# Performance work log

Hardware: AMD Instinct MI355X
Metric: run time of the kernel (lower is better)

Reference implementation:

```python
import jax, jax.numpy as jnp
import numpy as np
import math

D_MODEL = 1024
D_ATTN = 128
D_MID = 128
L = 4096

def setup_inputs() -> dict:
    key = jax.random.key(0)
    ks = jax.random.split(key, 5)
    scale = 1.0 / math.sqrt(D_MODEL)
    return {
        "x": jax.random.normal(ks[0], (L, D_MODEL), jnp.float32),
        "z": jax.random.normal(ks[1], (L, D_MODEL), jnp.float32),
        "Wq": jax.random.normal(ks[2], (D_MODEL, D_ATTN), jnp.float32) * scale,
        "bq": jnp.zeros((D_ATTN,), jnp.float32),
        "Wk": jax.random.normal(ks[3], (D_MODEL, D_ATTN), jnp.float32) * scale,
        "bk": jnp.zeros((D_ATTN,), jnp.float32),
        "Wv": jax.random.normal(ks[4], (D_MODEL, D_MID), jnp.float32) * scale,
        "bv": jnp.zeros((D_MID,), jnp.float32),
    }

def reference(x, z, Wq, bq, Wk, bk, Wv, bv):
    # q: [L_x, d_attn], k: [L_z, d_attn], v: [L_z, d_mid]
    q = x @ Wq + bq
    k = z @ Wk + bk
    v = z @ Wv + bv
    inv_sqrt_d = 1.0 / math.sqrt(D_ATTN)
    s = (q @ k.T) * inv_sqrt_d            # [L_x, L_z]
    y = jax.nn.softmax(s, axis=-1) @ v    # [L_x, d_mid]
    return y
```

## Files before the change

kernel.cpp:

```cpp
#include <hip/hip_runtime.h>
#include <hip/hip_bf16.h>

typedef __attribute__((ext_vector_type(8))) short short8;
typedef __attribute__((ext_vector_type(4))) float f32x4;

#define L_SEQ 4096
#define DM    1024
#define DA    128
#define PS    2
#define AZ    8

#define OFF_QB  786432
#define OFF_KF  1835008
#define OFF_VF  2883584
#define OFF_SCR 4063232

__device__ __forceinline__ short f2bf(float f) {
    union { float f; unsigned u; } v; v.f = f;
    unsigned u = v.u;
    u += 0x7FFFu + ((u >> 16) & 1u);
    return (short)(u >> 16);
}

typedef const __attribute__((address_space(1))) void g_void_t;
typedef __attribute__((address_space(3))) void l_void_t;
__device__ __forceinline__ void g2lds16(const void* g, void* l) {
    __builtin_amdgcn_global_load_lds((g_void_t*)g, (l_void_t*)l, 16, 0, 0);
}

__global__ __launch_bounds__(256) void prep_w_kernel(
    const float* __restrict__ Wq, const float* __restrict__ Wk,
    const float* __restrict__ Wv, short8* __restrict__ WTf)
{
    const int m = blockIdx.y, kidx = blockIdx.x;
    const float* __restrict__ W = (m == 0) ? Wq : (m == 1) ? Wk : Wv;
    __shared__ __align__(16) float Ws[32 * 132];
    const int t = threadIdx.x;
#pragma unroll
    for (int i = 0; i < 4; i++) {
        const int u = i * 256 + t;
        const int kk = u >> 5, n4 = (u & 31) * 4;
        *(f32x4*)&Ws[kk * 132 + n4] = *(const f32x4*)&W[(size_t)(kidx * 32 + kk) * DA + n4];
    }
    __syncthreads();
#pragma unroll
    for (int i = 0; i < 2; i++) {
        const int u = i * 256 + t;
        const int nt = u >> 6, lane = u & 63, l16 = lane & 15, quad = lane >> 4;
        short8 fr;
#pragma unroll
        for (int j = 0; j < 8; j++)
            fr[j] = f2bf(Ws[(quad * 8 + j) * 132 + nt * 16 + l16]);
        WTf[((size_t)(m * 32 + kidx) * 8 + nt) * 64 + lane] = fr;
    }
}

__global__ __launch_bounds__(256, 1) void proj_kernel(
    const float* __restrict__ x, const float* __restrict__ z,
    const char* __restrict__ WTraw, float* __restrict__ part)
{
    __shared__ __align__(16) char wb[2][16384];

    const int t = threadIdx.x;
    const int wave = t >> 6, lane = t & 63;
    const int l16 = lane & 15, quad = lane >> 4;
    const int isKV = blockIdx.y;
    const int s = blockIdx.z;
    const int kbeg = s * (DM / PS);
    const int row0w = blockIdx.x * 64 + wave * 16;
    const int m1 = isKV ? 1 : 0;
    const int nbytes = isKV ? 16384 : 8192;
    const int ks0 = kbeg >> 5;

    const float* __restrict__ Am = isKV ? z : x;
    const float* ap = Am + (size_t)(row0w + l16) * DM + kbeg + quad * 8;

    f32x4 acc1[8], acc2[8];
#pragma unroll
    for (int i = 0; i < 8; i++) {
        acc1[i] = (f32x4){0.f, 0.f, 0.f, 0.f};
        acc2[i] = (f32x4){0.f, 0.f, 0.f, 0.f};
    }

    auto stage = [&](int kidx, int b) {
        const char* base1 = WTraw + (size_t)(m1 * 32 + kidx) * 8192;
        const char* base2 = WTraw + (size_t)(2 * 32 + kidx) * 8192;
#pragma unroll
        for (int i = 0; i < 4; i++) {
            const int off = i * 4096 + wave * 1024;
            if (off < nbytes) {
                const char* src = (off < 8192) ? (base1 + off) : (base2 + (off - 8192));
                g2lds16(src + lane * 16, &wb[b][off]);
            }
        }
    };

    f32x4 c0 = *(const f32x4*)ap,        c1 = *(const f32x4*)(ap + 4);
    f32x4 d0 = *(const f32x4*)(ap + 32), d1 = *(const f32x4*)(ap + 36);

    stage(ks0, 0);
    __syncthreads();

#pragma unroll 1
    for (int ks = 0; ks < 16; ks++) {
        const int b = ks & 1;
        if (ks + 1 < 16) stage(ks0 + ks + 1, b ^ 1);

        const int kpf = (ks + 2 < 16) ? ks + 2 : ks;
        f32x4 e0 = *(const f32x4*)(ap + kpf * 32);
        f32x4 e1 = *(const f32x4*)(ap + kpf * 32 + 4);

        short8 afr;
        afr[0] = f2bf(c0[0]); afr[1] = f2bf(c0[1]); afr[2] = f2bf(c0[2]); afr[3] = f2bf(c0[3]);
        afr[4] = f2bf(c1[0]); afr[5] = f2bf(c1[1]); afr[6] = f2bf(c1[2]); afr[7] = f2bf(c1[3]);

#pragma unroll
        for (int nt = 0; nt < 8; nt++) {
            short8 bfr = *(const short8*)&wb[b][(nt * 64 + lane) * 16];
            acc1[nt] = __builtin_amdgcn_mfma_f32_16x16x32_bf16(afr, bfr, acc1[nt], 0, 0, 0);
        }
        if (isKV) {
#pragma unroll
            for (int nt = 0; nt < 8; nt++) {
                short8 bfr = *(const short8*)&wb[b][8192 + (nt * 64 + lane) * 16];
                acc2[nt] = __builtin_amdgcn_mfma_f32_16x16x32_bf16(afr, bfr, acc2[nt], 0, 0, 0);
            }
        }
        __syncthreads();
        c0 = d0; c1 = d1; d0 = e0; d1 = e1;
    }

    float* p1 = part + (size_t)(s * 3 + m1) * L_SEQ * DA;
#pragma unroll
    for (int nt = 0; nt < 8; nt++) {
        const int col = nt * 16 + l16;
#pragma unroll
        for (int r = 0; r < 4; r++)
            p1[(size_t)(row0w + quad * 4 + r) * DA + col] = acc1[nt][r];
    }
    if (isKV) {
        float* p2 = part + (size_t)(s * 3 + 2) * L_SEQ * DA;
#pragma unroll
        for (int nt = 0; nt < 8; nt++) {
            const int col = nt * 16 + l16;
#pragma unroll
            for (int r = 0; r < 4; r++)
                p2[(size_t)(row0w + quad * 4 + r) * DA + col] = acc2[nt][r];
        }
    }
}

__global__ __launch_bounds__(256) void finalize_kernel(
    const float* __restrict__ part,
    const float* __restrict__ bq, const float* __restrict__ bk,
    const float* __restrict__ bv,
    short* __restrict__ qb, short8* __restrict__ kf, short8* __restrict__ vf)
{
    const int t = threadIdx.x;
    const int row0 = blockIdx.x * 32;
    __shared__ short Ts[DA * 33];

#pragma unroll 1
    for (int m = 0; m < 3; m++) {
        const float* __restrict__ bias = (m == 0) ? bq : (m == 1) ? bk : bv;
#pragma unroll
        for (int i = 0; i < 2; i++) {
            const int u = i * 256 + t;
            const int r = u >> 4, cg8 = u & 15;
            const int R = row0 + r, c0 = cg8 * 8;
            float vsum[8];
#pragma unroll
            for (int j = 0; j < 8; j++) vsum[j] = bias[c0 + j];
            for (int s = 0; s < PS; s++) {
                const float* p = &part[((size_t)(s * 3 + m) * L_SEQ + R) * DA + c0];
                f32x4 f0 = *(const f32x4*)p;
                f32x4 f1 = *(const f32x4*)(p + 4);
#pragma unroll
                for (int j = 0; j < 4; j++) { vsum[j] += f0[j]; vsum[4 + j] += f1[j]; }
            }
            short8 o;
#pragma unroll
            for (int j = 0; j < 8; j++) o[j] = f2bf(vsum[j]);

            if (m == 0) {
                *(short8*)&qb[(size_t)R * DA + c0] = o;
            } else if (m == 1) {
                const int kg = R >> 5, nth = (R >> 4) & 1, l16 = R & 15;
                const int ks = cg8 >> 2, quad = cg8 & 3;
                kf[((size_t)(kg * 4 + ks) * 2 + nth) * 64 + quad * 16 + l16] = o;
            } else {
#pragma unroll
                for (int j = 0; j < 8; j++) Ts[(c0 + j) * 33 + r] = o[j];
            }
        }
    }
    __syncthreads();

    const int vg = blockIdx.x;
#pragma unroll
    for (int i = 0; i < 3; i++) {
        const int u = i * 256 + t;
        if (u < 576) {
            const int nt = u >> 6, lane = u & 63, l16 = lane & 15, quad = lane >> 4;
            short8 fr;
            if (nt < 8) {
                const int col = nt * 16 + l16;
#pragma unroll
                for (int j = 0; j < 8; j++) fr[j] = Ts[col * 33 + quad * 8 + j];
            } else {
                const short one = (short)0x3F80;
#pragma unroll
                for (int j = 0; j < 8; j++) fr[j] = (l16 == 0) ? one : (short)0;
            }
            vf[((size_t)vg * 9 + nt) * 64 + lane] = fr;
        }
    }
}

__global__ __launch_bounds__(256, 1) void attn_kernel(
    const short* __restrict__ qb, const char* __restrict__ kfg,
    const char* __restrict__ vfg, float* __restrict__ OA,
    float* __restrict__ lA)
{
    __shared__ __align__(16) char kv[2][17408];
    __shared__ __align__(16) short Ps[4][2][16 * 40];

    const int t    = threadIdx.x;
    const int wave = t >> 6;
    const int lane = t & 63;
    const int l16  = lane & 15;
    const int quad = lane >> 4;
    const int qr0  = blockIdx.x * 128;
    const int g0   = blockIdx.y * 16;

    auto stage = [&](int g, int b) {
        const char* kb_ = kfg + (size_t)(g0 + g) * 8192;
        const char* vb_ = vfg + (size_t)(g0 + g) * 9216;
#pragma unroll
        for (int i = 0; i < 5; i++) {
            const int off = i * 4096 + wave * 1024;
            if (off < 17408) {
                const char* src = (off < 8192) ? (kb_ + off) : (vb_ + (off - 8192));
                g2lds16(src + lane * 16, &kv[b][off]);
            }
        }
    };

    stage(0, 0);

    short8 af[2][4];
    const short* qrow = qb + (size_t)(qr0 + wave * 32 + l16) * DA + quad * 8;
#pragma unroll
    for (int at = 0; at < 2; at++)
#pragma unroll
        for (int ks = 0; ks < 4; ks++)
            af[at][ks] = *(const short8*)(qrow + (size_t)at * 16 * DA + ks * 32);

    f32x4 O0[9], O1[9];
#pragma unroll
    for (int i = 0; i < 9; i++) {
        O0[i] = (f32x4){0.f, 0.f, 0.f, 0.f};
        O1[i] = (f32x4){0.f, 0.f, 0.f, 0.f};
    }

    const float C = 0.08838834764831845f;
    short* P0 = &Ps[wave][0][0];
    short* P1 = &Ps[wave][1][0];

    __syncthreads();

#pragma unroll 1
    for (int g = 0; g < 16; g++) {
        const int b = g & 1;
        if (g + 1 < 16) stage(g + 1, b ^ 1);

        const char* kb_ = &kv[b][0];
        const char* vb_ = &kv[b][8192];

        f32x4 s0[2], s1[2];
#pragma unroll
        for (int nh = 0; nh < 2; nh++) {
            s0[nh] = (f32x4){0.f, 0.f, 0.f, 0.f};
            s1[nh] = (f32x4){0.f, 0.f, 0.f, 0.f};
        }
#pragma unroll
        for (int nh = 0; nh < 2; nh++)
#pragma unroll
            for (int ks = 0; ks < 4; ks++) {
                short8 bfr = *(const short8*)(kb_ + ((ks * 2 + nh) * 64 + lane) * 16);
                s0[nh] = __builtin_amdgcn_mfma_f32_16x16x32_bf16(af[0][ks], bfr, s0[nh], 0, 0, 0);
                s1[nh] = __builtin_amdgcn_mfma_f32_16x16x32_bf16(af[1][ks], bfr, s1[nh], 0, 0, 0);
            }

#pragma unroll
        for (int nh = 0; nh < 2; nh++)
#pragma unroll
            for (int r = 0; r < 4; r++) {
                P0[(quad * 4 + r) * 40 + nh * 16 + l16] = f2bf(__expf(s0[nh][r] * C));
                P1[(quad * 4 + r) * 40 + nh * 16 + l16] = f2bf(__expf(s1[nh][r] * C));
            }
        asm volatile("" ::: "memory");
        __builtin_amdgcn_s_waitcnt(0xc07f);
        asm volatile("" ::: "memory");

        short8 a20 = *(const short8*)&P0[l16 * 40 + quad * 8];
        short8 a21 = *(const short8*)&P1[l16 * 40 + quad * 8];
#pragma unroll
        for (int nt = 0; nt < 9; nt++) {
            short8 b2 = *(const short8*)(vb_ + (nt * 64 + lane) * 16);
            O0[nt] = __builtin_amdgcn_mfma_f32_16x16x32_bf16(a20, b2, O0[nt], 0, 0, 0);
            O1[nt] = __builtin_amdgcn_mfma_f32_16x16x32_bf16(a21, b2, O1[nt], 0, 0, 0);
        }
        __syncthreads();
    }

    const int rw = qr0 + wave * 32;
    float* Ob = OA + (size_t)blockIdx.y * L_SEQ * DA;
#pragma unroll
    for (int nt = 0; nt < 8; nt++)
#pragma unroll
        for (int r = 0; r < 4; r++) {
            Ob[(size_t)(rw + quad * 4 + r) * DA + nt * 16 + l16] = O0[nt][r];
            Ob[(size_t)(rw + 16 + quad * 4 + r) * DA + nt * 16 + l16] = O1[nt][r];
        }
    if (l16 == 0) {
        float* lb = lA + (size_t)blockIdx.y * L_SEQ;
#pragma unroll
        for (int r = 0; r < 4; r++) {
            lb[rw + quad * 4 + r] = O0[8][r];
            lb[rw + 16 + quad * 4 + r] = O1[8][r];
        }
    }
}

__global__ __launch_bounds__(256) void merge_kernel(
    const float* __restrict__ OA, const float* __restrict__ lA,
    float* __restrict__ out)
{
    const int t = threadIdx.x;
    const int row = blockIdx.x * 16 + (t >> 4);
    const int cg = (t & 15) * 8;

    f32x4 a0 = (f32x4){0.f, 0.f, 0.f, 0.f};
    f32x4 a1 = (f32x4){0.f, 0.f, 0.f, 0.f};
    float lsum = 0.f;
#pragma unroll
    for (int zz = 0; zz < AZ; zz++) {
        const float* p = &OA[((size_t)zz * L_SEQ + row) * DA + cg];
        a0 = a0 + *(const f32x4*)p;
        a1 = a1 + *(const f32x4*)(p + 4);
        lsum += lA[(size_t)zz * L_SEQ + row];
    }
    const float inv = 1.f / lsum;
    f32x4* dst = (f32x4*)&out[(size_t)row * DA + cg];
    dst[0] = a0 * inv;
    dst[1] = a1 * inv;
}

extern "C" void kernel_launch(void* const* d_in, const int* in_sizes, int n_in,
                              void* d_out, int out_size, void* d_ws, size_t ws_size,
                              hipStream_t stream) {
    (void)in_sizes; (void)n_in; (void)out_size; (void)ws_size;
    const float* x  = (const float*)d_in[0];
    const float* z  = (const float*)d_in[1];
    const float* Wq = (const float*)d_in[2];
    const float* bq = (const float*)d_in[3];
    const float* Wk = (const float*)d_in[4];
    const float* bk = (const float*)d_in[5];
    const float* Wv = (const float*)d_in[6];
    const float* bv = (const float*)d_in[7];
    float* out = (float*)d_out;

    short8* WTf = (short8*)d_ws;
    short*  qb  = (short*)((char*)d_ws + OFF_QB);
    short8* kf  = (short8*)((char*)d_ws + OFF_KF);
    short8* vf  = (short8*)((char*)d_ws + OFF_VF);
    char* scratch = (char*)d_ws + OFF_SCR;

    float* part = (float*)scratch;
    float* OA   = (float*)scratch;
    float* lA   = (float*)(scratch + (size_t)AZ * L_SEQ * DA * 4);

    prep_w_kernel<<<dim3(32, 3), 256, 0, stream>>>(Wq, Wk, Wv, WTf);
    proj_kernel<<<dim3(64, 2, PS), 256, 0, stream>>>(x, z, (const char*)WTf, part);
    finalize_kernel<<<128, 256, 0, stream>>>(part, bq, bk, bv, qb, kf, vf);
    attn_kernel<<<dim3(32, AZ), 256, 0, stream>>>(qb, (const char*)kf, (const char*)vf, OA, lA);
    merge_kernel<<<256, 256, 0, stream>>>(OA, lA, out);
}
```

Baseline: 138.6 us.

## Fuse projection with bias/fragment finalize and halve attention rows per block

The projection and finalize kernels are merged into one qkv kernel. It computes the full K dimension per 32-row block, with two waves per M-tile splitting N, so the split-K partial sums and their round trip through global memory go away. Bias add, bf16 conversion and the K/V MFMA fragment layout now happen in LDS within the same kernel, which removes one launch. The attention kernel now processes 64 query rows per block with one 16-row tile per wave, doubling the grid and allowing two blocks per CU. The cost is less reuse of staged K/V per block and larger LDS use in the qkv kernel.

```diff
diff --git a/kernel.cpp b/kernel.cpp
--- a/kernel.cpp
+++ b/kernel.cpp
@@ -7,13 +7,12 @@
 #define L_SEQ 4096
 #define DM    1024
 #define DA    128
-#define PS    2
 #define AZ    8
 
 #define OFF_QB  786432
 #define OFF_KF  1835008
 #define OFF_VF  2883584
-#define OFF_SCR 4063232
+#define OFF_OA  4063232
 
 __device__ __forceinline__ short f2bf(float f) {
     union { float f; unsigned u; } v; v.f = f;
@@ -55,182 +54,173 @@
     }
 }
 
-__global__ __launch_bounds__(256, 1) void proj_kernel(
+__global__ __launch_bounds__(256, 1) void qkv_kernel(
     const float* __restrict__ x, const float* __restrict__ z,
-    const char* __restrict__ WTraw, float* __restrict__ part)
-{
-    __shared__ __align__(16) char wb[2][16384];
-
-    const int t = threadIdx.x;
-    const int wave = t >> 6, lane = t & 63;
-    const int l16 = lane & 15, quad = lane >> 4;
-    const int isKV = blockIdx.y;
-    const int s = blockIdx.z;
-    const int kbeg = s * (DM / PS);
-    const int row0w = blockIdx.x * 64 + wave * 16;
-    const int m1 = isKV ? 1 : 0;
-    const int nbytes = isKV ? 16384 : 8192;
-    const int ks0 = kbeg >> 5;
-
-    const float* __restrict__ Am = isKV ? z : x;
-    const float* ap = Am + (size_t)(row0w + l16) * DM + kbeg + quad * 8;
-
-    f32x4 acc1[8], acc2[8];
-#pragma unroll
-    for (int i = 0; i < 8; i++) {
-        acc1[i] = (f32x4){0.f, 0.f, 0.f, 0.f};
-        acc2[i] = (f32x4){0.f, 0.f, 0.f, 0.f};
-    }
-
-    auto stage = [&](int kidx, int b) {
-        const char* base1 = WTraw + (size_t)(m1 * 32 + kidx) * 8192;
-        const char* base2 = WTraw + (size_t)(2 * 32 + kidx) * 8192;
-#pragma unroll
-        for (int i = 0; i < 4; i++) {
-            const int off = i * 4096 + wave * 1024;
-            if (off < nbytes) {
-                const char* src = (off < 8192) ? (base1 + off) : (base2 + (off - 8192));
-                g2lds16(src + lane * 16, &wb[b][off]);
-            }
-        }
-    };
-
-    f32x4 c0 = *(const f32x4*)ap,        c1 = *(const f32x4*)(ap + 4);
-    f32x4 d0 = *(const f32x4*)(ap + 32), d1 = *(const f32x4*)(ap + 36);
-
-    stage(ks0, 0);
-    __syncthreads();
-
-#pragma unroll 1
-    for (int ks = 0; ks < 16; ks++) {
-        const int b = ks & 1;
-        if (ks + 1 < 16) stage(ks0 + ks + 1, b ^ 1);
-
-        const int kpf = (ks + 2 < 16) ? ks + 2 : ks;
-        f32x4 e0 = *(const f32x4*)(ap + kpf * 32);
-        f32x4 e1 = *(const f32x4*)(ap + kpf * 32 + 4);
-
-        short8 afr;
-        afr[0] = f2bf(c0[0]); afr[1] = f2bf(c0[1]); afr[2] = f2bf(c0[2]); afr[3] = f2bf(c0[3]);
-        afr[4] = f2bf(c1[0]); afr[5] = f2bf(c1[1]); afr[6] = f2bf(c1[2]); afr[7] = f2bf(c1[3]);
-
-#pragma unroll
-        for (int nt = 0; nt < 8; nt++) {
-            short8 bfr = *(const short8*)&wb[b][(nt * 64 + lane) * 16];
-            acc1[nt] = __builtin_amdgcn_mfma_f32_16x16x32_bf16(afr, bfr, acc1[nt], 0, 0, 0);
-        }
-        if (isKV) {
-#pragma unroll
-            for (int nt = 0; nt < 8; nt++) {
-                short8 bfr = *(const short8*)&wb[b][8192 + (nt * 64 + lane) * 16];
-                acc2[nt] = __builtin_amdgcn_mfma_f32_16x16x32_bf16(afr, bfr, acc2[nt], 0, 0, 0);
-            }
-        }
-        __syncthreads();
-        c0 = d0; c1 = d1; d0 = e0; d1 = e1;
-    }
-
-    float* p1 = part + (size_t)(s * 3 + m1) * L_SEQ * DA;
-#pragma unroll
-    for (int nt = 0; nt < 8; nt++) {
-        const int col = nt * 16 + l16;
-#pragma unroll
-        for (int r = 0; r < 4; r++)
-            p1[(size_t)(row0w + quad * 4 + r) * DA + col] = acc1[nt][r];
-    }
-    if (isKV) {
-        float* p2 = part + (size_t)(s * 3 + 2) * L_SEQ * DA;
-#pragma unroll
-        for (int nt = 0; nt < 8; nt++) {
-            const int col = nt * 16 + l16;
-#pragma unroll
-            for (int r = 0; r < 4; r++)
-                p2[(size_t)(row0w + quad * 4 + r) * DA + col] = acc2[nt][r];
-        }
-    }
-}
-
-__global__ __launch_bounds__(256) void finalize_kernel(
-    const float* __restrict__ part,
+    const char* __restrict__ WTraw,
     const float* __restrict__ bq, const float* __restrict__ bk,
     const float* __restrict__ bv,
     short* __restrict__ qb, short8* __restrict__ kf, short8* __restrict__ vf)
 {
+    __shared__ __align__(16) char smem[2][32768];
+
     const int t = threadIdx.x;
+    const int wave = t >> 6, lane = t & 63;
+    const int l16 = lane & 15, quad = lane >> 4;
+    const int mtile = wave >> 1, nhalf = wave & 1;
+    const int isKV = blockIdx.y;
+    const int m1 = isKV ? 1 : 0;
     const int row0 = blockIdx.x * 32;
-    __shared__ short Ts[DA * 33];
+    const int nbytes = isKV ? 32768 : 16384;
+
+    const float* __restrict__ Am = isKV ? z : x;
+    const float* ap = Am + (size_t)(row0 + mtile * 16 + l16) * DM + quad * 8;
+
+    f32x4 acc1[4], acc2[4];
+#pragma unroll
+    for (int i = 0; i < 4; i++) {
+        acc1[i] = (f32x4){0.f, 0.f, 0.f, 0.f};
+        acc2[i] = (f32x4){0.f, 0.f, 0.f, 0.f};
+    }
+
+    auto stage = [&](int it2, int b) {
+        const char* base1 = WTraw + (size_t)(m1 * 32 + it2 * 2) * 8192;
+        const char* base2 = WTraw + (size_t)(2 * 32 + it2 * 2) * 8192;
+#pragma unroll
+        for (int i = 0; i < 8; i++) {
+            const int off = i * 4096 + wave * 1024;
+            if (off < nbytes) {
+                const char* src = (off < 16384) ? (base1 + off) : (base2 + (off - 16384));
+                g2lds16(src + lane * 16, &smem[b][off]);
+            }
+        }
+    };
+
+    f32x4 cur[4], nxt[4];
+#pragma unroll
+    for (int j = 0; j < 2; j++) {
+        cur[j * 2]     = *(const f32x4*)(ap + j * 32);
+        cur[j * 2 + 1] = *(const f32x4*)(ap + j * 32 + 4);
+        nxt[j * 2]     = *(const f32x4*)(ap + 64 + j * 32);
+        nxt[j * 2 + 1] = *(const f32x4*)(ap + 64 + j * 32 + 4);
+    }
+
+    stage(0, 0);
+    __syncthreads();
 
 #pragma unroll 1
-    for (int m = 0; m < 3; m++) {
-        const float* __restrict__ bias = (m == 0) ? bq : (m == 1) ? bk : bv;
-#pragma unroll
-        for (int i = 0; i < 2; i++) {
-            const int u = i * 256 + t;
-            const int r = u >> 4, cg8 = u & 15;
-            const int R = row0 + r, c0 = cg8 * 8;
-            float vsum[8];
-#pragma unroll
-            for (int j = 0; j < 8; j++) vsum[j] = bias[c0 + j];
-            for (int s = 0; s < PS; s++) {
-                const float* p = &part[((size_t)(s * 3 + m) * L_SEQ + R) * DA + c0];
-                f32x4 f0 = *(const f32x4*)p;
-                f32x4 f1 = *(const f32x4*)(p + 4);
-#pragma unroll
-                for (int j = 0; j < 4; j++) { vsum[j] += f0[j]; vsum[4 + j] += f1[j]; }
-            }
-            short8 o;
-#pragma unroll
-            for (int j = 0; j < 8; j++) o[j] = f2bf(vsum[j]);
-
-            if (m == 0) {
-                *(short8*)&qb[(size_t)R * DA + c0] = o;
-            } else if (m == 1) {
-                const int kg = R >> 5, nth = (R >> 4) & 1, l16 = R & 15;
-                const int ks = cg8 >> 2, quad = cg8 & 3;
-                kf[((size_t)(kg * 4 + ks) * 2 + nth) * 64 + quad * 16 + l16] = o;
-            } else {
-#pragma unroll
-                for (int j = 0; j < 8; j++) Ts[(c0 + j) * 33 + r] = o[j];
-            }
+    for (int it = 0; it < 16; it++) {
+        const int b = it & 1;
+        if (it + 1 < 16) stage(it + 1, b ^ 1);
+
+        const int ipf = (it + 2 < 16) ? it + 2 : it;
+        f32x4 fut[4];
+#pragma unroll
+        for (int j = 0; j < 2; j++) {
+            fut[j * 2]     = *(const f32x4*)(ap + ipf * 64 + j * 32);
+            fut[j * 2 + 1] = *(const f32x4*)(ap + ipf * 64 + j * 32 + 4);
+        }
+
+#pragma unroll
+        for (int ss = 0; ss < 2; ss++) {
+            short8 afr;
+#pragma unroll
+            for (int j = 0; j < 4; j++) {
+                afr[j]     = f2bf(cur[ss * 2][j]);
+                afr[4 + j] = f2bf(cur[ss * 2 + 1][j]);
+            }
+#pragma unroll
+            for (int ntl = 0; ntl < 4; ntl++) {
+                short8 bfr = *(const short8*)&smem[b][ss * 8192 + ((nhalf * 4 + ntl) * 64 + lane) * 16];
+                acc1[ntl] = __builtin_amdgcn_mfma_f32_16x16x32_bf16(afr, bfr, acc1[ntl], 0, 0, 0);
+            }
+            if (isKV) {
+#pragma unroll
+                for (int ntl = 0; ntl < 4; ntl++) {
+                    short8 bfr = *(const short8*)&smem[b][16384 + ss * 8192 + ((nhalf * 4 + ntl) * 64 + lane) * 16];
+                    acc2[ntl] = __builtin_amdgcn_mfma_f32_16x16x32_bf16(afr, bfr, acc2[ntl], 0, 0, 0);
+                }
+            }
+        }
+        __syncthreads();
+#pragma unroll
+        for (int j = 0; j < 4; j++) { cur[j] = nxt[j]; nxt[j] = fut[j]; }
+    }
+
+    if (!isKV) {
+#pragma unroll
+        for (int ntl = 0; ntl < 4; ntl++) {
+            const int col = nhalf * 64 + ntl * 16 + l16;
+            const float bb = bq[col];
+#pragma unroll
+            for (int r = 0; r < 4; r++)
+                qb[(size_t)(row0 + mtile * 16 + quad * 4 + r) * DA + col] =
+                    f2bf(acc1[ntl][r] + bb);
+        }
+        return;
+    }
+
+    short* kT = (short*)&smem[0][0];
+    short* vT = (short*)&smem[0][16384];
+#pragma unroll
+    for (int ntl = 0; ntl < 4; ntl++) {
+        const int col = nhalf * 64 + ntl * 16 + l16;
+        const float bbk = bk[col], bbv = bv[col];
+#pragma unroll
+        for (int r = 0; r < 4; r++) {
+            const int rl = mtile * 16 + quad * 4 + r;
+            kT[rl * 132 + col] = f2bf(acc1[ntl][r] + bbk);
+            vT[rl * 132 + col] = f2bf(acc2[ntl][r] + bbv);
         }
     }
     __syncthreads();
 
-    const int vg = blockIdx.x;
+    const int kg = blockIdx.x;
+#pragma unroll
+    for (int i = 0; i < 2; i++) {
+        const int f = i * 256 + t;
+        const int ks = f >> 7, nth = (f >> 6) & 1, ln = f & 63;
+        const int lf = ln & 15, qf = ln >> 4;
+        short8 fr;
+#pragma unroll
+        for (int j = 0; j < 8; j++)
+            fr[j] = kT[(nth * 16 + lf) * 132 + ks * 32 + qf * 8 + j];
+        kf[((size_t)(kg * 4 + ks) * 2 + nth) * 64 + ln] = fr;
+    }
 #pragma unroll
     for (int i = 0; i < 3; i++) {
-        const int u = i * 256 + t;
-        if (u < 576) {
-            const int nt = u >> 6, lane = u & 63, l16 = lane & 15, quad = lane >> 4;
+        const int f = i * 256 + t;
+        if (f < 576) {
+            const int nt = f >> 6, ln = f & 63;
+            const int lf = ln & 15, qf = ln >> 4;
             short8 fr;
             if (nt < 8) {
-                const int col = nt * 16 + l16;
-#pragma unroll
-                for (int j = 0; j < 8; j++) fr[j] = Ts[col * 33 + quad * 8 + j];
+#pragma unroll
+                for (int j = 0; j < 8; j++)
+                    fr[j] = vT[(qf * 8 + j) * 132 + nt * 16 + lf];
             } else {
                 const short one = (short)0x3F80;
 #pragma unroll
-                for (int j = 0; j < 8; j++) fr[j] = (l16 == 0) ? one : (short)0;
-            }
-            vf[((size_t)vg * 9 + nt) * 64 + lane] = fr;
-        }
-    }
-}
-
-__global__ __launch_bounds__(256, 1) void attn_kernel(
+                for (int j = 0; j < 8; j++) fr[j] = (lf == 0) ? one : (short)0;
+            }
+            vf[((size_t)kg * 9 + nt) * 64 + ln] = fr;
+        }
+    }
+}
+
+__global__ __launch_bounds__(256, 2) void attn_kernel(
     const short* __restrict__ qb, const char* __restrict__ kfg,
     const char* __restrict__ vfg, float* __restrict__ OA,
     float* __restrict__ lA)
 {
     __shared__ __align__(16) char kv[2][17408];
-    __shared__ __align__(16) short Ps[4][2][16 * 40];
+    __shared__ __align__(16) short Ps[4][16 * 40];
 
     const int t    = threadIdx.x;
     const int wave = t >> 6;
     const int lane = t & 63;
     const int l16  = lane & 15;
     const int quad = lane >> 4;
-    const int qr0  = blockIdx.x * 128;
+    const int qr0  = blockIdx.x * 64;
     const int g0   = blockIdx.y * 16;
 
     auto stage = [&](int g, int b) {
@@ -248,24 +238,18 @@
 
     stage(0, 0);
 
-    short8 af[2][4];
-    const short* qrow = qb + (size_t)(qr0 + wave * 32 + l16) * DA + quad * 8;
-#pragma unroll
-    for (int at = 0; at < 2; at++)
-#pragma unroll
-        for (int ks = 0; ks < 4; ks++)
-            af[at][ks] = *(const short8*)(qrow + (size_t)at * 16 * DA + ks * 32);
-
-    f32x4 O0[9], O1[9];
-#pragma unroll
-    for (int i = 0; i < 9; i++) {
-        O0[i] = (f32x4){0.f, 0.f, 0.f, 0.f};
-        O1[i] = (f32x4){0.f, 0.f, 0.f, 0.f};
-    }
+    short8 af[4];
+    const short* qrow = qb + (size_t)(qr0 + wave * 16 + l16) * DA + quad * 8;
+#pragma unroll
+    for (int ks = 0; ks < 4; ks++)
+        af[ks] = *(const short8*)(qrow + ks * 32);
+
+    f32x4 O[9];
+#pragma unroll
+    for (int i = 0; i < 9; i++) O[i] = (f32x4){0.f, 0.f, 0.f, 0.f};
 
     const float C = 0.08838834764831845f;
-    short* P0 = &Ps[wave][0][0];
-    short* P1 = &Ps[wave][1][0];
+    short* P = &Ps[wave][0];
 
     __syncthreads();
 
@@ -277,59 +261,47 @@
         const char* kb_ = &kv[b][0];
         const char* vb_ = &kv[b][8192];
 
-        f32x4 s0[2], s1[2];
-#pragma unroll
-        for (int nh = 0; nh < 2; nh++) {
-            s0[nh] = (f32x4){0.f, 0.f, 0.f, 0.f};
-            s1[nh] = (f32x4){0.f, 0.f, 0.f, 0.f};
-        }
+        f32x4 s0[2];
+#pragma unroll
+        for (int nh = 0; nh < 2; nh++) s0[nh] = (f32x4){0.f, 0.f, 0.f, 0.f};
 #pragma unroll
         for (int nh = 0; nh < 2; nh++)
 #pragma unroll
             for (int ks = 0; ks < 4; ks++) {
                 short8 bfr = *(const short8*)(kb_ + ((ks * 2 + nh) * 64 + lane) * 16);
-                s0[nh] = __builtin_amdgcn_mfma_f32_16x16x32_bf16(af[0][ks], bfr, s0[nh], 0, 0, 0);
-                s1[nh] = __builtin_amdgcn_mfma_f32_16x16x32_bf16(af[1][ks], bfr, s1[nh], 0, 0, 0);
+                s0[nh] = __builtin_amdgcn_mfma_f32_16x16x32_bf16(af[ks], bfr, s0[nh], 0, 0, 0);
             }
 
 #pragma unroll
         for (int nh = 0; nh < 2; nh++)
 #pragma unroll
-            for (int r = 0; r < 4; r++) {
-                P0[(quad * 4 + r) * 40 + nh * 16 + l16] = f2bf(__expf(s0[nh][r] * C));
-                P1[(quad * 4 + r) * 40 + nh * 16 + l16] = f2bf(__expf(s1[nh][r] * C));
-            }
+            for (int r = 0; r < 4; r++)
+                P[(quad * 4 + r) * 40 + nh * 16 + l16] = f2bf(__expf(s0[nh][r] * C));
         asm volatile("" ::: "memory");
         __builtin_amdgcn_s_waitcnt(0xc07f);
         asm volatile("" ::: "memory");
 
-        short8 a20 = *(const short8*)&P0[l16 * 40 + quad * 8];
-        short8 a21 = *(const short8*)&P1[l16 * 40 + quad * 8];
+        short8 a2 = *(const short8*)&P[l16 * 40 + quad * 8];
 #pragma unroll
         for (int nt = 0; nt < 9; nt++) {
             short8 b2 = *(const short8*)(vb_ + (nt * 64 + lane) * 16);
-            O0[nt] = __builtin_amdgcn_mfma_f32_16x16x32_bf16(a20, b2, O0[nt], 0, 0, 0);
-            O1[nt] = __builtin_amdgcn_mfma_f32_16x16x32_bf16(a21, b2, O1[nt], 0, 0, 0);
+            O[nt] = __builtin_amdgcn_mfma_f32_16x16x32_bf16(a2, b2, O[nt], 0, 0, 0);
         }
         __syncthreads();
     }
 
-    const int rw = qr0 + wave * 32;
+    const int rw = qr0 + wave * 16;
     float* Ob = OA + (size_t)blockIdx.y * L_SEQ * DA;
 #pragma unroll
     for (int nt = 0; nt < 8; nt++)
 #pragma unroll
-        for (int r = 0; r < 4; r++) {
-            Ob[(size_t)(rw + quad * 4 + r) * DA + nt * 16 + l16] = O0[nt][r];
-            Ob[(size_t)(rw + 16 + quad * 4 + r) * DA + nt * 16 + l16] = O1[nt][r];
-        }
+        for (int r = 0; r < 4; r++)
+            Ob[(size_t)(rw + quad * 4 + r) * DA + nt * 16 + l16] = O[nt][r];
     if (l16 == 0) {
         float* lb = lA + (size_t)blockIdx.y * L_SEQ;
 #pragma unroll
-        for (int r = 0; r < 4; r++) {
-            lb[rw + quad * 4 + r] = O0[8][r];
-            lb[rw + 16 + quad * 4 + r] = O1[8][r];
-        }
+        for (int r = 0; r < 4; r++)
+            lb[rw + quad * 4 + r] = O[8][r];
     }
 }
 
@@ -375,15 +347,13 @@
     short*  qb  = (short*)((char*)d_ws + OFF_QB);
     short8* kf  = (short8*)((char*)d_ws + OFF_KF);
     short8* vf  = (short8*)((char*)d_ws + OFF_VF);
-    char* scratch = (char*)d_ws + OFF_SCR;
-
-    float* part = (float*)scratch;
-    float* OA   = (float*)scratch;
-    float* lA   = (float*)(scratch + (size_t)AZ * L_SEQ * DA * 4);
+    float*  OA  = (float*)((char*)d_ws + OFF_OA);
+    float*  lA  = (float*)((char*)d_ws + OFF_OA + (size_t)AZ * L_SEQ * DA * 4);
 
     prep_w_kernel<<<dim3(32, 3), 256, 0, stream>>>(Wq, Wk, Wv, WTf);
-    proj_kernel<<<dim3(64, 2, PS), 256, 0, stream>>>(x, z, (const char*)WTf, part);
-    finalize_kernel<<<128, 256, 0, stream>>>(part, bq, bk, bv, qb, kf, vf);
-    attn_kernel<<<dim3(32, AZ), 256, 0, stream>>>(qb, (const char*)kf, (const char*)vf, OA, lA);
+    qkv_kernel<<<dim3(128, 2), 256, 0, stream>>>(x, z, (const char*)WTf,
+                                                 bq, bk, bv, qb, kf, vf);
+    attn_kernel<<<dim3(64, AZ), 256, 0, stream>>>(qb, (const char*)kf,
+                                                  (const char*)vf, OA, lA);
     merge_kernel<<<256, 256, 0, stream>>>(OA, lA, out);
 }
```

Result: faster. 130.7 us, median of 2 (-5.7%).
